# Performance work log

Hardware: AMD Instinct MI355X
Metric: run time of the kernel (lower is better)

The kernel has to match this reference:

```python
import jax, jax.numpy as jnp
import numpy as np

N, C_IN, H, W = 1024, 22, 19, 19
C_TRUNK, HID, NHIST = 384, 128, 5
HIST_START = 9  # channels 9..13 hold move history planes


def setup_inputs() -> dict:
    key = jax.random.key(0)
    ks = jax.random.split(key, 8)
    return {
        "input_spatial": jax.random.uniform(ks[0], (N, C_IN, H, W), dtype=jnp.float32),
        "trunk_out": jax.random.normal(ks[1], (N, C_TRUNK, H, W), dtype=jnp.float32),
        "w_ih": jax.random.normal(ks[2], (4 * HID, C_TRUNK), dtype=jnp.float32) * 0.05,
        "w_hh": jax.random.normal(ks[3], (4 * HID, HID), dtype=jnp.float32) * 0.05,
        "b_ih": jax.random.normal(ks[4], (4 * HID,), dtype=jnp.float32) * 0.05,
        "b_hh": jax.random.normal(ks[5], (4 * HID,), dtype=jnp.float32) * 0.05,
        "w_proj": jax.random.normal(ks[6], (C_TRUNK, HID), dtype=jnp.float32) * 0.05,
        "b_proj": jax.random.normal(ks[7], (C_TRUNK,), dtype=jnp.float32) * 0.05,
    }


def reference(input_spatial, trunk_out, w_ih, w_hh, b_ih, b_hh, w_proj, b_proj):
    n, _, h, w = input_spatial.shape
    c_trunk = trunk_out.shape[1]
    # --- extract_move_coords (vectorized) ---
    planes = input_spatial[:, HIST_START:HIST_START + NHIST]          # N,5,H,W
    flat = planes.reshape(n, NHIST, h * w)                            # N,5,HW
    has_move = flat.sum(axis=-1) > 0.5                                # N,5 bool
    idx = jnp.argmax(flat, axis=-1)                                   # N,5 (== r*W+c; clamp(-1,min=0)==0 handled by mask)
    # --- gather trunk features at move coords, mask missing moves ---
    trunk_flat = trunk_out.reshape(n, c_trunk, h * w)                 # N,Ct,HW
    feats = jnp.take_along_axis(trunk_flat, idx[:, None, :], axis=2)  # N,Ct,5
    feats = feats.transpose(0, 2, 1) * has_move[..., None].astype(trunk_out.dtype)  # N,5,Ct
    seq = feats[:, ::-1, :]                                           # oldest -> newest
    # --- single-layer LSTM (torch gate order: i, f, g, o) ---
    def step(carry, x_t):
        h_t, c_t = carry
        g = x_t @ w_ih.T + h_t @ w_hh.T + b_ih + b_hh                 # N,4H
        i_g, f_g, g_g, o_g = jnp.split(g, 4, axis=-1)
        c_new = jax.nn.sigmoid(f_g) * c_t + jax.nn.sigmoid(i_g) * jnp.tanh(g_g)
        h_new = jax.nn.sigmoid(o_g) * jnp.tanh(c_new)
        return (h_new, c_new), None

    h0 = jnp.zeros((n, HID), dtype=seq.dtype)
    (h_final, _), _ = jax.lax.scan(step, (h0, h0), seq.transpose(1, 0, 2))
    out = h_final @ w_proj.T + b_proj                                 # N,Ct
    return out[:, :, None, None]                                      # N,Ct,1,1
```

## Files before the change

### kernel.cpp

```cpp
#include <hip/hip_runtime.h>
#include <hip/hip_bf16.h>
#include <float.h>

#define N_SAMP   1024
#define C_IN     22
#define HW       361
#define C_TRUNK  384
#define HID      128
#define NHIST    5
#define HIST_START 9
#define NGATE    512

typedef __attribute__((ext_vector_type(8))) short short8v;
typedef __attribute__((ext_vector_type(4))) float float4v;

static __device__ __forceinline__ ushort f2bf(float x) {
  unsigned int b = __float_as_uint(x);
  b += 0x7fffu + ((b >> 16) & 1u);
  return (ushort)(b >> 16);
}

__global__ __launch_bounds__(320) void argmax_kernel(
    const float* __restrict__ inp,
    const float* __restrict__ w_ih,
    int*    __restrict__ idxb,
    float*  __restrict__ movb,
    ushort* __restrict__ w_ihb)
{
  const int n    = blockIdx.x;
  const int tid  = threadIdx.x;
  const int wave = tid >> 6;
  const int lane = tid & 63;

  if (n < 768 && tid < 256) {
    int o = n * 256 + tid;
    w_ihb[o] = f2bf(w_ih[o]);
  }

  const float* base = inp + ((size_t)n * C_IN + HIST_START + wave) * HW;
  float v = -FLT_MAX; int vi = 0; float sum = 0.f;
  #pragma unroll
  for (int r = 0; r < 6; ++r) {
    int i = lane + r * 64;
    if (i < HW) {
      float x = base[i];
      sum += x;
      if (x > v) { v = x; vi = i; }
    }
  }
  #pragma unroll
  for (int m = 1; m < 64; m <<= 1) {
    float v2 = __shfl_xor(v, m);
    int   i2 = __shfl_xor(vi, m);
    float s2 = __shfl_xor(sum, m);
    if (v2 > v || (v2 == v && i2 < vi)) { v = v2; vi = i2; }
    sum += s2;
  }
  if (lane == 0) {
    idxb[n * NHIST + wave] = vi;
    movb[n * NHIST + wave] = (sum > 0.5f) ? 1.f : 0.f;
  }
}

__global__ __launch_bounds__(192) void gather_kernel(
    const float* __restrict__ trunk,
    const int*   __restrict__ idxb,
    const float* __restrict__ movb,
    ushort* __restrict__ seq)
{
  const int n = blockIdx.x;
  const int c = threadIdx.x;

  const int   i0 = idxb[n * NHIST + 4], i1 = idxb[n * NHIST + 3],
              i2 = idxb[n * NHIST + 2], i3 = idxb[n * NHIST + 1],
              i4 = idxb[n * NHIST + 0];
  const float m0 = movb[n * NHIST + 4], m1 = movb[n * NHIST + 3],
              m2 = movb[n * NHIST + 2], m3 = movb[n * NHIST + 1],
              m4 = movb[n * NHIST + 0];

  const float* ta = trunk + ((size_t)n * C_TRUNK + c) * HW;
  const float* tb = ta + (size_t)192 * HW;
  float a0 = ta[i0], a1 = ta[i1], a2 = ta[i2], a3 = ta[i3], a4 = ta[i4];
  float b0 = tb[i0], b1 = tb[i1], b2 = tb[i2], b3 = tb[i3], b4 = tb[i4];

  ushort* so = seq + (size_t)n * NHIST * C_TRUNK + c;
  so[0 * C_TRUNK]       = f2bf(a0 * m0);
  so[1 * C_TRUNK]       = f2bf(a1 * m1);
  so[2 * C_TRUNK]       = f2bf(a2 * m2);
  so[3 * C_TRUNK]       = f2bf(a3 * m3);
  so[4 * C_TRUNK]       = f2bf(a4 * m4);
  so[0 * C_TRUNK + 192] = f2bf(b0 * m0);
  so[1 * C_TRUNK + 192] = f2bf(b1 * m1);
  so[2 * C_TRUNK + 192] = f2bf(b2 * m2);
  so[3 * C_TRUNK + 192] = f2bf(b3 * m3);
  so[4 * C_TRUNK + 192] = f2bf(b4 * m4);
}

__global__ __launch_bounds__(256) void gates_kernel(
    const ushort* __restrict__ seq,
    const ushort* __restrict__ w_ihb,
    const float*  __restrict__ b_ih,
    const float*  __restrict__ b_hh,
    float* __restrict__ G)
{
  __shared__ ushort As[64][40];
  __shared__ ushort Bs[64][40];
  const int tid  = threadIdx.x;
  const int wv   = tid >> 6;
  const int lane = tid & 63;
  const int m0 = blockIdx.y * 64;
  const int j0 = blockIdx.x * 64;
  const int row_l = tid >> 2;
  const int koff  = (tid & 3) * 8;

  float4v acc0 = {0.f,0.f,0.f,0.f};
  float4v acc1 = {0.f,0.f,0.f,0.f};
  float4v acc2 = {0.f,0.f,0.f,0.f};
  float4v acc3 = {0.f,0.f,0.f,0.f};

  const int fr = lane & 15;
  const int fk = (lane >> 4) * 8;

  for (int k0 = 0; k0 < C_TRUNK; k0 += 32) {
    *(short8v*)&As[row_l][koff] =
        *(const short8v*)(seq + (size_t)(m0 + row_l) * C_TRUNK + k0 + koff);
    *(short8v*)&Bs[row_l][koff] =
        *(const short8v*)(w_ihb + (size_t)(j0 + row_l) * C_TRUNK + k0 + koff);
    __syncthreads();

    short8v af  = *(const short8v*)&As[wv * 16 + fr][fk];
    short8v bf0 = *(const short8v*)&Bs[ 0 + fr][fk];
    short8v bf1 = *(const short8v*)&Bs[16 + fr][fk];
    short8v bf2 = *(const short8v*)&Bs[32 + fr][fk];
    short8v bf3 = *(const short8v*)&Bs[48 + fr][fk];
    acc0 = __builtin_amdgcn_mfma_f32_16x16x32_bf16(af, bf0, acc0, 0, 0, 0);
    acc1 = __builtin_amdgcn_mfma_f32_16x16x32_bf16(af, bf1, acc1, 0, 0, 0);
    acc2 = __builtin_amdgcn_mfma_f32_16x16x32_bf16(af, bf2, acc2, 0, 0, 0);
    acc3 = __builtin_amdgcn_mfma_f32_16x16x32_bf16(af, bf3, acc3, 0, 0, 0);
    __syncthreads();
  }

  const int rbase = m0 + wv * 16 + (lane >> 4) * 4;
  #pragma unroll
  for (int j = 0; j < 4; ++j) {
    const float4v a = (j == 0) ? acc0 : (j == 1) ? acc1 : (j == 2) ? acc2 : acc3;
    const int cj = j0 + j * 16 + fr;
    const float bsum = b_ih[cj] + b_hh[cj];
    #pragma unroll
    for (int r = 0; r < 4; ++r)
      G[(size_t)(rbase + r) * NGATE + cj] = a[r] + bsum;
  }
}

__global__ __launch_bounds__(512, 2) void lstm_kernel(
    const float* __restrict__ G,
    const float* __restrict__ w_hh,
    const float* __restrict__ w_proj,
    const float* __restrict__ b_proj,
    float* __restrict__ out)
{
  const int n0   = blockIdx.x * 4;
  const int tid  = threadIdx.x;
  const int wv   = tid >> 6;
  const int lane = tid & 63;
  const int fr   = lane & 15;
  const int fq   = lane >> 4;

  __shared__ ushort hswz[4][64][8];
  __shared__ float  glds[NGATE][4];

  ((ushort4*)hswz)[tid] = make_ushort4(0, 0, 0, 0);

  const int j0w = wv * 64;
  short8v bfrag[4][4];
  #pragma unroll
  for (int f = 0; f < 4; ++f)
    #pragma unroll
    for (int ks = 0; ks < 4; ++ks) {
      const float* wr = w_hh + (size_t)(j0w + f*16 + fr) * HID + ks*32 + fq*8;
      float4 lo = *(const float4*)wr;
      float4 hi = *(const float4*)(wr + 4);
      short8v b;
      b[0]=(short)f2bf(lo.x); b[1]=(short)f2bf(lo.y);
      b[2]=(short)f2bf(lo.z); b[3]=(short)f2bf(lo.w);
      b[4]=(short)f2bf(hi.x); b[5]=(short)f2bf(hi.y);
      b[6]=(short)f2bf(hi.z); b[7]=(short)f2bf(hi.w);
      bfrag[f][ks] = b;
    }

  float4v gpre[NHIST][4];
  #pragma unroll
  for (int t = 0; t < NHIST; ++t)
    #pragma unroll
    for (int f = 0; f < 4; ++f) {
      float4v v = {0.f, 0.f, 0.f, 0.f};
      if (fq == 0) {
        const int col = j0w + f*16 + fr;
        #pragma unroll
        for (int r = 0; r < 4; ++r)
          v[r] = G[((size_t)(n0 + r) * NHIST + t) * NGATE + col];
      }
      gpre[t][f] = v;
    }

  float c4[4] = {0.f, 0.f, 0.f, 0.f};
  __syncthreads();

  #pragma unroll
  for (int t = 0; t < NHIST; ++t) {
    short8v af0 = *(const short8v*)&hswz[0][lane][0];
    short8v af1 = *(const short8v*)&hswz[1][lane][0];
    short8v af2 = *(const short8v*)&hswz[2][lane][0];
    short8v af3 = *(const short8v*)&hswz[3][lane][0];
    #pragma unroll
    for (int f = 0; f < 4; ++f) {
      float4v acc = gpre[t][f];
      acc = __builtin_amdgcn_mfma_f32_16x16x32_bf16(af0, bfrag[f][0], acc, 0, 0, 0);
      acc = __builtin_amdgcn_mfma_f32_16x16x32_bf16(af1, bfrag[f][1], acc, 0, 0, 0);
      acc = __builtin_amdgcn_mfma_f32_16x16x32_bf16(af2, bfrag[f][2], acc, 0, 0, 0);
      acc = __builtin_amdgcn_mfma_f32_16x16x32_bf16(af3, bfrag[f][3], acc, 0, 0, 0);
      if (fq == 0)
        *(float4v*)&glds[j0w + f*16 + fr][0] = acc;
    }
    __syncthreads();

    if (tid < HID) {
      const int j = tid;
      float4 iv = *(const float4*)&glds[      j][0];
      float4 fv = *(const float4*)&glds[128 + j][0];
      float4 gv = *(const float4*)&glds[256 + j][0];
      float4 ov = *(const float4*)&glds[384 + j][0];
      float ia[4] = {iv.x, iv.y, iv.z, iv.w};
      float fa[4] = {fv.x, fv.y, fv.z, fv.w};
      float ga[4] = {gv.x, gv.y, gv.z, gv.w};
      float oa[4] = {ov.x, ov.y, ov.z, ov.w};
      #pragma unroll
      for (int s = 0; s < 4; ++s) {
        float ig = 1.f / (1.f + __expf(-ia[s]));
        float fg = 1.f / (1.f + __expf(-fa[s]));
        float og = 1.f / (1.f + __expf(-oa[s]));
        c4[s] = fg * c4[s] + ig * tanhf(ga[s]);
        float h = og * tanhf(c4[s]);
        hswz[j >> 5][((j >> 3) & 3) * 16 + s][j & 7] = f2bf(h);
      }
    }
    __syncthreads();
  }

  const int j0p = wv * 48;
  short8v pfrag[3][4];
  #pragma unroll
  for (int f = 0; f < 3; ++f)
    #pragma unroll
    for (int ks = 0; ks < 4; ++ks) {
      const float* wr = w_proj + (size_t)(j0p + f*16 + fr) * HID + ks*32 + fq*8;
      float4 lo = *(const float4*)wr;
      float4 hi = *(const float4*)(wr + 4);
      short8v b;
      b[0]=(short)f2bf(lo.x); b[1]=(short)f2bf(lo.y);
      b[2]=(short)f2bf(lo.z); b[3]=(short)f2bf(lo.w);
      b[4]=(short)f2bf(hi.x); b[5]=(short)f2bf(hi.y);
      b[6]=(short)f2bf(hi.z); b[7]=(short)f2bf(hi.w);
      pfrag[f][ks] = b;
    }

  short8v hf0 = *(const short8v*)&hswz[0][lane][0];
  short8v hf1 = *(const short8v*)&hswz[1][lane][0];
  short8v hf2 = *(const short8v*)&hswz[2][lane][0];
  short8v hf3 = *(const short8v*)&hswz[3][lane][0];
  #pragma unroll
  for (int f = 0; f < 3; ++f) {
    const int col = j0p + f * 16 + fr;
    const float bp = b_proj[col];
    float4v acc = {bp, bp, bp, bp};
    acc = __builtin_amdgcn_mfma_f32_16x16x32_bf16(hf0, pfrag[f][0], acc, 0, 0, 0);
    acc = __builtin_amdgcn_mfma_f32_16x16x32_bf16(hf1, pfrag[f][1], acc, 0, 0, 0);
    acc = __builtin_amdgcn_mfma_f32_16x16x32_bf16(hf2, pfrag[f][2], acc, 0, 0, 0);
    acc = __builtin_amdgcn_mfma_f32_16x16x32_bf16(hf3, pfrag[f][3], acc, 0, 0, 0);
    if (fq == 0) {
      #pragma unroll
      for (int r = 0; r < 4; ++r)
        out[(size_t)(n0 + r) * C_TRUNK + col] = acc[r];
    }
  }
}

extern "C" void kernel_launch(void* const* d_in, const int* in_sizes, int n_in,
                              void* d_out, int out_size, void* d_ws, size_t ws_size,
                              hipStream_t stream) {
  const float* inp    = (const float*)d_in[0];
  const float* trunk  = (const float*)d_in[1];
  const float* w_ih   = (const float*)d_in[2];
  const float* w_hh   = (const float*)d_in[3];
  const float* b_ih   = (const float*)d_in[4];
  const float* b_hh   = (const float*)d_in[5];
  const float* w_proj = (const float*)d_in[6];
  const float* b_proj = (const float*)d_in[7];
  float* out = (float*)d_out;

  char* ws = (char*)d_ws;
  int*    idxb  = (int*)ws;
  float*  movb  = (float*)(ws + 20480);
  ushort* w_ihb = (ushort*)(ws + 40960);
  ushort* seq   = (ushort*)(ws + 40960 + 393216);
  float*  G     = (float*)(ws + 40960 + 393216 +
                   (size_t)N_SAMP * NHIST * C_TRUNK * sizeof(ushort));

  argmax_kernel<<<N_SAMP, 320, 0, stream>>>(inp, w_ih, idxb, movb, w_ihb);
  gather_kernel<<<N_SAMP, 192, 0, stream>>>(trunk, idxb, movb, seq);
  gates_kernel<<<dim3(NGATE / 64, (N_SAMP * NHIST) / 64), 256, 0, stream>>>(
      seq, w_ihb, b_ih, b_hh, G);
  lstm_kernel<<<N_SAMP / 4, 512, 0, stream>>>(G, w_hh, w_proj, b_proj, out);
}
```

Before: 77.87 us.

## Fuse argmax and gather into one prep kernel; store gate preactivations as bf16

Merges the argmax and gather kernels into a single prep kernel that passes move indices and masks through shared memory instead of global buffers. This removes one launch and a global round trip. The precomputed input-gate matrix G is also written as bf16 instead of fp32, halving its write traffic in gates_kernel and its read traffic in lstm_kernel. The cost is lower precision on the gate preactivations before the recurrent MFMA accumulation.

```diff
diff --git a/kernel.cpp b/kernel.cpp
--- a/kernel.cpp
+++ b/kernel.cpp
@@ -19,81 +19,80 @@
   b += 0x7fffu + ((b >> 16) & 1u);
   return (ushort)(b >> 16);
 }
-
-__global__ __launch_bounds__(320) void argmax_kernel(
+static __device__ __forceinline__ float bf2f(ushort u) {
+  return __uint_as_float(((unsigned int)u) << 16);
+}
+
+__global__ __launch_bounds__(384) void prep_kernel(
     const float* __restrict__ inp,
     const float* __restrict__ w_ih,
-    int*    __restrict__ idxb,
-    float*  __restrict__ movb,
-    ushort* __restrict__ w_ihb)
+    const float* __restrict__ trunk,
+    ushort* __restrict__ w_ihb,
+    ushort* __restrict__ seq)
 {
   const int n    = blockIdx.x;
   const int tid  = threadIdx.x;
   const int wave = tid >> 6;
   const int lane = tid & 63;
+  __shared__ int   s_idx[NHIST];
+  __shared__ float s_mov[NHIST];
 
   if (n < 768 && tid < 256) {
     int o = n * 256 + tid;
     w_ihb[o] = f2bf(w_ih[o]);
   }
 
-  const float* base = inp + ((size_t)n * C_IN + HIST_START + wave) * HW;
-  float v = -FLT_MAX; int vi = 0; float sum = 0.f;
-  #pragma unroll
-  for (int r = 0; r < 6; ++r) {
-    int i = lane + r * 64;
-    if (i < HW) {
-      float x = base[i];
-      sum += x;
-      if (x > v) { v = x; vi = i; }
-    }
-  }
-  #pragma unroll
-  for (int m = 1; m < 64; m <<= 1) {
-    float v2 = __shfl_xor(v, m);
-    int   i2 = __shfl_xor(vi, m);
-    float s2 = __shfl_xor(sum, m);
-    if (v2 > v || (v2 == v && i2 < vi)) { v = v2; vi = i2; }
-    sum += s2;
-  }
-  if (lane == 0) {
-    idxb[n * NHIST + wave] = vi;
-    movb[n * NHIST + wave] = (sum > 0.5f) ? 1.f : 0.f;
-  }
-}
-
-__global__ __launch_bounds__(192) void gather_kernel(
-    const float* __restrict__ trunk,
-    const int*   __restrict__ idxb,
-    const float* __restrict__ movb,
-    ushort* __restrict__ seq)
-{
-  const int n = blockIdx.x;
-  const int c = threadIdx.x;
-
-  const int   i0 = idxb[n * NHIST + 4], i1 = idxb[n * NHIST + 3],
-              i2 = idxb[n * NHIST + 2], i3 = idxb[n * NHIST + 1],
-              i4 = idxb[n * NHIST + 0];
-  const float m0 = movb[n * NHIST + 4], m1 = movb[n * NHIST + 3],
-              m2 = movb[n * NHIST + 2], m3 = movb[n * NHIST + 1],
-              m4 = movb[n * NHIST + 0];
-
-  const float* ta = trunk + ((size_t)n * C_TRUNK + c) * HW;
-  const float* tb = ta + (size_t)192 * HW;
-  float a0 = ta[i0], a1 = ta[i1], a2 = ta[i2], a3 = ta[i3], a4 = ta[i4];
-  float b0 = tb[i0], b1 = tb[i1], b2 = tb[i2], b3 = tb[i3], b4 = tb[i4];
-
-  ushort* so = seq + (size_t)n * NHIST * C_TRUNK + c;
-  so[0 * C_TRUNK]       = f2bf(a0 * m0);
-  so[1 * C_TRUNK]       = f2bf(a1 * m1);
-  so[2 * C_TRUNK]       = f2bf(a2 * m2);
-  so[3 * C_TRUNK]       = f2bf(a3 * m3);
-  so[4 * C_TRUNK]       = f2bf(a4 * m4);
-  so[0 * C_TRUNK + 192] = f2bf(b0 * m0);
-  so[1 * C_TRUNK + 192] = f2bf(b1 * m1);
-  so[2 * C_TRUNK + 192] = f2bf(b2 * m2);
-  so[3 * C_TRUNK + 192] = f2bf(b3 * m3);
-  so[4 * C_TRUNK + 192] = f2bf(b4 * m4);
+  if (wave < NHIST) {
+    const float* base = inp + ((size_t)n * C_IN + HIST_START + wave) * HW;
+    float v = -FLT_MAX; int vi = 0; float sum = 0.f;
+    #pragma unroll
+    for (int r = 0; r < 6; ++r) {
+      int i = lane + r * 64;
+      if (i < HW) {
+        float x = base[i];
+        sum += x;
+        if (x > v) { v = x; vi = i; }
+      }
+    }
+    #pragma unroll
+    for (int m = 1; m < 64; m <<= 1) {
+      float v2 = __shfl_xor(v, m);
+      int   i2 = __shfl_xor(vi, m);
+      float s2 = __shfl_xor(sum, m);
+      if (v2 > v || (v2 == v && i2 < vi)) { v = v2; vi = i2; }
+      sum += s2;
+    }
+    if (lane == 0) {
+      s_idx[wave] = vi;
+      s_mov[wave] = (sum > 0.5f) ? 1.f : 0.f;
+    }
+  }
+  __syncthreads();
+
+  if (tid < 192) {
+    const int c = tid;
+    const int   i0 = s_idx[4], i1 = s_idx[3], i2 = s_idx[2],
+                i3 = s_idx[1], i4 = s_idx[0];
+    const float m0 = s_mov[4], m1 = s_mov[3], m2 = s_mov[2],
+                m3 = s_mov[1], m4 = s_mov[0];
+
+    const float* ta = trunk + ((size_t)n * C_TRUNK + c) * HW;
+    const float* tb = ta + (size_t)192 * HW;
+    float a0 = ta[i0], a1 = ta[i1], a2 = ta[i2], a3 = ta[i3], a4 = ta[i4];
+    float b0 = tb[i0], b1 = tb[i1], b2 = tb[i2], b3 = tb[i3], b4 = tb[i4];
+
+    ushort* so = seq + (size_t)n * NHIST * C_TRUNK + c;
+    so[0 * C_TRUNK]       = f2bf(a0 * m0);
+    so[1 * C_TRUNK]       = f2bf(a1 * m1);
+    so[2 * C_TRUNK]       = f2bf(a2 * m2);
+    so[3 * C_TRUNK]       = f2bf(a3 * m3);
+    so[4 * C_TRUNK]       = f2bf(a4 * m4);
+    so[0 * C_TRUNK + 192] = f2bf(b0 * m0);
+    so[1 * C_TRUNK + 192] = f2bf(b1 * m1);
+    so[2 * C_TRUNK + 192] = f2bf(b2 * m2);
+    so[3 * C_TRUNK + 192] = f2bf(b3 * m3);
+    so[4 * C_TRUNK + 192] = f2bf(b4 * m4);
+  }
 }
 
 __global__ __launch_bounds__(256) void gates_kernel(
@@ -101,7 +100,7 @@
     const ushort* __restrict__ w_ihb,
     const float*  __restrict__ b_ih,
     const float*  __restrict__ b_hh,
-    float* __restrict__ G)
+    ushort* __restrict__ G)
 {
   __shared__ ushort As[64][40];
   __shared__ ushort Bs[64][40];
@@ -148,12 +147,12 @@
     const float bsum = b_ih[cj] + b_hh[cj];
     #pragma unroll
     for (int r = 0; r < 4; ++r)
-      G[(size_t)(rbase + r) * NGATE + cj] = a[r] + bsum;
+      G[(size_t)(rbase + r) * NGATE + cj] = f2bf(a[r] + bsum);
   }
 }
 
 __global__ __launch_bounds__(512, 2) void lstm_kernel(
-    const float* __restrict__ G,
+    const ushort* __restrict__ G,
     const float* __restrict__ w_hh,
     const float* __restrict__ w_proj,
     const float* __restrict__ b_proj,
@@ -198,7 +197,7 @@
         const int col = j0w + f*16 + fr;
         #pragma unroll
         for (int r = 0; r < 4; ++r)
-          v[r] = G[((size_t)(n0 + r) * NHIST + t) * NGATE + col];
+          v[r] = bf2f(G[((size_t)(n0 + r) * NHIST + t) * NGATE + col]);
       }
       gpre[t][f] = v;
     }
@@ -299,15 +298,11 @@
   float* out = (float*)d_out;
 
   char* ws = (char*)d_ws;
-  int*    idxb  = (int*)ws;
-  float*  movb  = (float*)(ws + 20480);
-  ushort* w_ihb = (ushort*)(ws + 40960);
-  ushort* seq   = (ushort*)(ws + 40960 + 393216);
-  float*  G     = (float*)(ws + 40960 + 393216 +
-                   (size_t)N_SAMP * NHIST * C_TRUNK * sizeof(ushort));
-
-  argmax_kernel<<<N_SAMP, 320, 0, stream>>>(inp, w_ih, idxb, movb, w_ihb);
-  gather_kernel<<<N_SAMP, 192, 0, stream>>>(trunk, idxb, movb, seq);
+  ushort* w_ihb = (ushort*)ws;
+  ushort* seq   = (ushort*)(ws + 393216);
+  ushort* G     = (ushort*)(ws + 393216 + 3932160);
+
+  prep_kernel<<<N_SAMP, 384, 0, stream>>>(inp, w_ih, trunk, w_ihb, seq);
   gates_kernel<<<dim3(NGATE / 64, (N_SAMP * NHIST) / 64), 256, 0, stream>>>(
       seq, w_ihb, b_ih, b_hh, G);
   lstm_kernel<<<N_SAMP / 4, 512, 0, stream>>>(G, w_hh, w_proj, b_proj, out);
```

Result: no change. 78.46 us (+0.7%).
